# Optimization experiments

Measured on AMD Instinct MI355X. Metric: run time of the kernel, lower is better.

The kernel has to match this reference:

```python
import jax, jax.numpy as jnp
import numpy as np

TWO_PI = 6.283185  # constant used verbatim in the original module


def setup_inputs() -> dict:
    key = jax.random.key(0)
    ks = jax.random.split(key, 12)
    N, input_size, light_freq, H = 8388608, 11, 16, 16
    d_in = input_size - 2 + 2 * light_freq  # 41
    x = jax.random.uniform(ks[0], (N, input_size), dtype=jnp.float32)
    B_light = jax.random.normal(ks[1], (2, light_freq), dtype=jnp.float32)
    W1 = jax.random.normal(ks[2], (d_in, H), dtype=jnp.float32) * (1.0 / np.sqrt(d_in))
    b1 = jax.random.normal(ks[3], (H,), dtype=jnp.float32) * 0.01
    W2 = jax.random.normal(ks[4], (H, H), dtype=jnp.float32) * 0.25
    b2 = jax.random.normal(ks[5], (H,), dtype=jnp.float32) * 0.01
    W3 = jax.random.normal(ks[6], (H, H), dtype=jnp.float32) * 0.25
    b3 = jax.random.normal(ks[7], (H,), dtype=jnp.float32) * 0.01
    W4 = jax.random.normal(ks[8], (H, H), dtype=jnp.float32) * 0.25
    b4 = jax.random.normal(ks[9], (H,), dtype=jnp.float32) * 0.01
    W5 = jax.random.normal(ks[10], (H, 1), dtype=jnp.float32) * 0.25
    b5 = jax.random.normal(ks[11], (1,), dtype=jnp.float32) * 0.01
    return {"x": x, "B_light": B_light, "W1": W1, "b1": b1, "W2": W2, "b2": b2,
            "W3": W3, "b3": b3, "W4": W4, "b4": b4, "W5": W5, "b5": b5}


def reference(x, B_light, W1, b1, W2, b2, W3, b3, W4, b4, W5, b5):
    # Fourier-feature encoding of the last two input dims (light direction)
    x_light = TWO_PI * (x[:, -2:] @ B_light)                      # [N, F]
    feats = jnp.concatenate([x[:, :-2], jnp.cos(x_light), jnp.sin(x_light)], axis=-1)  # [N, 41]
    # Tiny 5-layer MLP with ELU activations
    h = jax.nn.elu(feats @ W1 + b1)
    h = jax.nn.elu(h @ W2 + b2)
    h = jax.nn.elu(h @ W3 + b3)
    h = jax.nn.elu(h @ W4 + b4)
    out = h @ W5 + b5                                             # [N, 1]
    return out
```

## Files before the change

kernel.cpp:

```cpp
#include <hip/hip_runtime.h>

typedef __fp16   cvt16x2 __attribute__((ext_vector_type(2)));
typedef _Float16 h2      __attribute__((ext_vector_type(2)));
typedef _Float16 half4_t __attribute__((ext_vector_type(4)));
typedef unsigned uint2v  __attribute__((ext_vector_type(2)));
typedef float    f32x4   __attribute__((ext_vector_type(4)));

#define CH 4

#if !__has_builtin(__builtin_elementwise_exp2)
extern "C" __device__ _Float16 __ocml_exp2_f16(_Float16);
#endif

__device__ __forceinline__ unsigned pk(float a, float b) {
    cvt16x2 h = __builtin_amdgcn_cvt_pkrtz(a, b);
    return __builtin_bit_cast(unsigned, h);
}
__device__ __forceinline__ half4_t mkfrag(unsigned lo, unsigned hi) {
    uint2v u; u[0] = lo; u[1] = hi;
    return __builtin_bit_cast(half4_t, u);
}

__device__ __forceinline__ unsigned elu_pk(float a, float b) {
    h2 v = __builtin_bit_cast(h2, __builtin_amdgcn_cvt_pkrtz(a, b));
    const h2 z  = {(_Float16)0.f, (_Float16)0.f};
    const h2 lg = {(_Float16)1.44269504f, (_Float16)1.44269504f};
    const h2 m1 = {(_Float16)-1.f, (_Float16)-1.f};
    h2 mx = __builtin_elementwise_max(v, z);
    h2 mn = __builtin_elementwise_min(v, z);
    h2 tt = mn * lg;
#if __has_builtin(__builtin_elementwise_exp2)
    h2 ev = __builtin_elementwise_exp2(tt);
#else
    h2 ev; ev[0] = __ocml_exp2_f16(tt[0]); ev[1] = __ocml_exp2_f16(tt[1]);
#endif
    h2 r = mx + (ev + m1);
    return __builtin_bit_cast(unsigned, r);
}

__device__ __forceinline__ float hdot2(unsigned a, unsigned b, float c) {
#if __has_builtin(__builtin_amdgcn_fdot2)
    return __builtin_amdgcn_fdot2(__builtin_bit_cast(cvt16x2, a),
                                  __builtin_bit_cast(cvt16x2, b), c, false);
#else
    h2 av = __builtin_bit_cast(h2, a), bv = __builtin_bit_cast(h2, b);
    return fmaf((float)av[1], (float)bv[1], fmaf((float)av[0], (float)bv[0], c));
#endif
}

__global__ __launch_bounds__(128, 4) void pixenc_mfma5(
    const float* __restrict__ x,
    const float* __restrict__ Bl,
    const float* __restrict__ W1, const float* __restrict__ b1,
    const float* __restrict__ W2, const float* __restrict__ b2,
    const float* __restrict__ W3, const float* __restrict__ b3,
    const float* __restrict__ W4, const float* __restrict__ b4,
    const float* __restrict__ W5, const float* __restrict__ b5,
    float* __restrict__ out, int N)
{
    const int t    = threadIdx.x;
    const int lane = t & 63;
    const int w    = t >> 6;
    const int g    = lane >> 4;
    const int m    = lane & 15;

    half4_t A1[3], A2, A3, A4;
    #pragma unroll
    for (int e = 0; e < 4; ++e) {
        const int c0 = 4 * e + g;
        A1[0][e] = (c0 < 9) ? (_Float16)W1[c0 * 16 + m] : (_Float16)0.f;
        A1[1][e] = (_Float16)W1[(9  + g * 4 + e) * 16 + m];
        A1[2][e] = (_Float16)W1[(25 + g * 4 + e) * 16 + m];
        A2[e]    = (_Float16)W2[(g * 4 + e) * 16 + m];
        A3[e]    = (_Float16)W3[(g * 4 + e) * 16 + m];
        A4[e]    = (_Float16)W4[(g * 4 + e) * 16 + m];
    }
    f32x4 c1, c2, c3, c4;
    float blc[4], bls[4];
    #pragma unroll
    for (int e = 0; e < 4; ++e) {
        const int r = g * 4 + e;
        c1[e] = b1[r]; c2[e] = b2[r]; c3[e] = b3[r]; c4[e] = b4[r];
        blc[e] = Bl[r]; bls[e] = Bl[16 + r];
    }
    const unsigned w5p0 = pk(W5[g * 4 + 0], W5[g * 4 + 1]);
    const unsigned w5p1 = pk(W5[g * 4 + 2], W5[g * 4 + 3]);
    const float b5v = b5[0];

    const int wavebase = blockIdx.x * (128 * CH) + w * (64 * CH);

    float xg0[4], xg1[4], x8v[4], x9v[4], x10v[4];
    #pragma unroll
    for (int s = 0; s < 4; ++s) {
        int j = wavebase + s * 16 + m; if (j >= N) j = N - 1;
        const float* rb = x + (size_t)j * 11;
        xg0[s] = rb[g];  xg1[s] = rb[4 + g];
        x8v[s] = rb[8];  x9v[s] = rb[9];  x10v[s] = rb[10];
    }

    #pragma unroll
    for (int c = 0; c < CH; ++c) {
        const int sbase = wavebase + c * 64;

        float ng0[4], ng1[4], n8[4], n9[4], n10[4];
        if (c + 1 < CH) {
            #pragma unroll
            for (int s = 0; s < 4; ++s) {
                int j = sbase + 64 + s * 16 + m; if (j >= N) j = N - 1;
                const float* rb = x + (size_t)j * 11;
                ng0[s] = rb[g];  ng1[s] = rb[4 + g];
                n8[s]  = rb[8];  n9[s]  = rb[9];  n10[s] = rb[10];
            }
        }

        f32x4 acc[4];
        #pragma unroll
        for (int s = 0; s < 4; ++s) {
            float cs[4], sn[4];
            #pragma unroll
            for (int e = 0; e < 4; ++e) {
                float zz = fmaf(x9v[s], blc[e], x10v[s] * bls[e]);
                zz = __builtin_amdgcn_fractf(zz);
                cs[e] = __builtin_amdgcn_cosf(zz);
                sn[e] = __builtin_amdgcn_sinf(zz);
            }
            const half4_t F0 = mkfrag(pk(xg0[s], xg1[s]), pk(x8v[s], 0.f));
            const half4_t F1 = mkfrag(pk(cs[0], cs[1]), pk(cs[2], cs[3]));
            const half4_t F2 = mkfrag(pk(sn[0], sn[1]), pk(sn[2], sn[3]));
            f32x4 a = c1;
            a = __builtin_amdgcn_mfma_f32_16x16x16f16(A1[0], F0, a, 0, 0, 0);
            a = __builtin_amdgcn_mfma_f32_16x16x16f16(A1[1], F1, a, 0, 0, 0);
            a = __builtin_amdgcn_mfma_f32_16x16x16f16(A1[2], F2, a, 0, 0, 0);
            acc[s] = a;
        }

        half4_t H[4];
        #pragma unroll
        for (int s = 0; s < 4; ++s)
            H[s] = mkfrag(elu_pk(acc[s][0], acc[s][1]), elu_pk(acc[s][2], acc[s][3]));
        #pragma unroll
        for (int s = 0; s < 4; ++s)
            acc[s] = __builtin_amdgcn_mfma_f32_16x16x16f16(A2, H[s], c2, 0, 0, 0);

        #pragma unroll
        for (int s = 0; s < 4; ++s)
            H[s] = mkfrag(elu_pk(acc[s][0], acc[s][1]), elu_pk(acc[s][2], acc[s][3]));
        #pragma unroll
        for (int s = 0; s < 4; ++s)
            acc[s] = __builtin_amdgcn_mfma_f32_16x16x16f16(A3, H[s], c3, 0, 0, 0);

        #pragma unroll
        for (int s = 0; s < 4; ++s)
            H[s] = mkfrag(elu_pk(acc[s][0], acc[s][1]), elu_pk(acc[s][2], acc[s][3]));
        #pragma unroll
        for (int s = 0; s < 4; ++s)
            acc[s] = __builtin_amdgcn_mfma_f32_16x16x16f16(A4, H[s], c4, 0, 0, 0);

        #pragma unroll
        for (int s = 0; s < 4; ++s) {
            const unsigned u0 = elu_pk(acc[s][0], acc[s][1]);
            const unsigned u1 = elu_pk(acc[s][2], acc[s][3]);
            float p = hdot2(u1, w5p1, hdot2(u0, w5p0, 0.f));
            p += __shfl_xor(p, 16, 64);
            p += __shfl_xor(p, 32, 64);
            const int o = sbase + s * 16 + m;
            if (g == 0 && o < N) out[o] = p + b5v;
        }

        if (c + 1 < CH) {
            #pragma unroll
            for (int s = 0; s < 4; ++s) {
                xg0[s] = ng0[s]; xg1[s] = ng1[s];
                x8v[s] = n8[s];  x9v[s] = n9[s];  x10v[s] = n10[s];
            }
        }
    }
}

extern "C" void kernel_launch(void* const* d_in, const int* in_sizes, int n_in,
                              void* d_out, int out_size, void* d_ws, size_t ws_size,
                              hipStream_t stream) {
    const float* x  = (const float*)d_in[0];
    const float* Bl = (const float*)d_in[1];
    const float* W1 = (const float*)d_in[2];
    const float* b1 = (const float*)d_in[3];
    const float* W2 = (const float*)d_in[4];
    const float* b2 = (const float*)d_in[5];
    const float* W3 = (const float*)d_in[6];
    const float* b3 = (const float*)d_in[7];
    const float* W4 = (const float*)d_in[8];
    const float* b4 = (const float*)d_in[9];
    const float* W5 = (const float*)d_in[10];
    const float* b5 = (const float*)d_in[11];
    float* out = (float*)d_out;

    const int N = out_size;
    const int blocks = (N + 128 * CH - 1) / (128 * CH);
    pixenc_mfma5<<<blocks, 128, 0, stream>>>(x, Bl, W1, b1, W2, b2, W3, b3,
                                             W4, b4, W5, b5, out, N);
}
```

Measured before the change: 144.9 us.

## Remove bounds checks via tail kernel, coalesce output stores, double chunk count

The main kernel now runs only on full blocks without per-row clamping, and a separate scalar kernel handles the remainder. Input addressing becomes strided pointer increments, and inputs are packed to fp16 at load time. After the shuffle reduction, each lane picks one sub-tile's result so all 64 lanes write one contiguous output instead of a quarter of lanes writing. ELU is simplified to max(v, exp(min(v,0))-1), and CH doubles to 8, halving the grid and amortising the weight setup per block at the cost of less parallelism.

```diff
diff --git a/kernel.cpp b/kernel.cpp
--- a/kernel.cpp
+++ b/kernel.cpp
@@ -6,7 +6,7 @@
 typedef unsigned uint2v  __attribute__((ext_vector_type(2)));
 typedef float    f32x4   __attribute__((ext_vector_type(4)));
 
-#define CH 4
+#define CH 8
 
 #if !__has_builtin(__builtin_elementwise_exp2)
 extern "C" __device__ _Float16 __ocml_exp2_f16(_Float16);
@@ -26,15 +26,13 @@
     const h2 z  = {(_Float16)0.f, (_Float16)0.f};
     const h2 lg = {(_Float16)1.44269504f, (_Float16)1.44269504f};
     const h2 m1 = {(_Float16)-1.f, (_Float16)-1.f};
-    h2 mx = __builtin_elementwise_max(v, z);
-    h2 mn = __builtin_elementwise_min(v, z);
-    h2 tt = mn * lg;
+    h2 t = __builtin_elementwise_min(v, z) * lg;
 #if __has_builtin(__builtin_elementwise_exp2)
-    h2 ev = __builtin_elementwise_exp2(tt);
+    h2 ev = __builtin_elementwise_exp2(t);
 #else
-    h2 ev; ev[0] = __ocml_exp2_f16(tt[0]); ev[1] = __ocml_exp2_f16(tt[1]);
+    h2 ev; ev[0] = __ocml_exp2_f16(t[0]); ev[1] = __ocml_exp2_f16(t[1]);
 #endif
-    h2 r = mx + (ev + m1);
+    h2 r = __builtin_elementwise_max(v, ev + m1);
     return __builtin_bit_cast(unsigned, r);
 }
 
@@ -48,7 +46,7 @@
 #endif
 }
 
-__global__ __launch_bounds__(128, 4) void pixenc_mfma5(
+__global__ __launch_bounds__(128, 4) void pixenc_mfma6(
     const float* __restrict__ x,
     const float* __restrict__ Bl,
     const float* __restrict__ W1, const float* __restrict__ b1,
@@ -56,7 +54,7 @@
     const float* __restrict__ W3, const float* __restrict__ b3,
     const float* __restrict__ W4, const float* __restrict__ b4,
     const float* __restrict__ W5, const float* __restrict__ b5,
-    float* __restrict__ out, int N)
+    float* __restrict__ out)
 {
     const int t    = threadIdx.x;
     const int lane = t & 63;
@@ -89,27 +87,32 @@
 
     const int wavebase = blockIdx.x * (128 * CH) + w * (64 * CH);
 
-    float xg0[4], xg1[4], x8v[4], x9v[4], x10v[4];
+    const float* aA = x + (size_t)(wavebase + m) * 11 + g;
+    const float* aB = x + (size_t)(wavebase + m) * 11 + 8;
+    float* outp = out + wavebase + lane;
+
+    unsigned cp0[4], cp8[4];
+    float cx9[4], cx10[4];
     #pragma unroll
     for (int s = 0; s < 4; ++s) {
-        int j = wavebase + s * 16 + m; if (j >= N) j = N - 1;
-        const float* rb = x + (size_t)j * 11;
-        xg0[s] = rb[g];  xg1[s] = rb[4 + g];
-        x8v[s] = rb[8];  x9v[s] = rb[9];  x10v[s] = rb[10];
+        const float a0 = aA[s * 176], a1 = aA[s * 176 + 4];
+        const float b8 = aB[s * 176], b9 = aB[s * 176 + 1], b10 = aB[s * 176 + 2];
+        cp0[s] = pk(a0, a1); cp8[s] = pk(b8, 0.f);
+        cx9[s] = b9; cx10[s] = b10;
     }
 
     #pragma unroll
     for (int c = 0; c < CH; ++c) {
-        const int sbase = wavebase + c * 64;
-
-        float ng0[4], ng1[4], n8[4], n9[4], n10[4];
+        unsigned np0[4], np8[4];
+        float nx9[4], nx10[4];
         if (c + 1 < CH) {
+            aA += 704; aB += 704;
             #pragma unroll
             for (int s = 0; s < 4; ++s) {
-                int j = sbase + 64 + s * 16 + m; if (j >= N) j = N - 1;
-                const float* rb = x + (size_t)j * 11;
-                ng0[s] = rb[g];  ng1[s] = rb[4 + g];
-                n8[s]  = rb[8];  n9[s]  = rb[9];  n10[s] = rb[10];
+                const float a0 = aA[s * 176], a1 = aA[s * 176 + 4];
+                const float b8 = aB[s * 176], b9 = aB[s * 176 + 1], b10 = aB[s * 176 + 2];
+                np0[s] = pk(a0, a1); np8[s] = pk(b8, 0.f);
+                nx9[s] = b9; nx10[s] = b10;
             }
         }
 
@@ -119,12 +122,12 @@
             float cs[4], sn[4];
             #pragma unroll
             for (int e = 0; e < 4; ++e) {
-                float zz = fmaf(x9v[s], blc[e], x10v[s] * bls[e]);
+                float zz = fmaf(cx9[s], blc[e], cx10[s] * bls[e]);
                 zz = __builtin_amdgcn_fractf(zz);
                 cs[e] = __builtin_amdgcn_cosf(zz);
                 sn[e] = __builtin_amdgcn_sinf(zz);
             }
-            const half4_t F0 = mkfrag(pk(xg0[s], xg1[s]), pk(x8v[s], 0.f));
+            const half4_t F0 = mkfrag(cp0[s], cp8[s]);
             const half4_t F1 = mkfrag(pk(cs[0], cs[1]), pk(cs[2], cs[3]));
             const half4_t F2 = mkfrag(pk(sn[0], sn[1]), pk(sn[2], sn[3]));
             f32x4 a = c1;
@@ -156,25 +159,72 @@
         for (int s = 0; s < 4; ++s)
             acc[s] = __builtin_amdgcn_mfma_f32_16x16x16f16(A4, H[s], c4, 0, 0, 0);
 
+        float p[4];
         #pragma unroll
         for (int s = 0; s < 4; ++s) {
             const unsigned u0 = elu_pk(acc[s][0], acc[s][1]);
             const unsigned u1 = elu_pk(acc[s][2], acc[s][3]);
-            float p = hdot2(u1, w5p1, hdot2(u0, w5p0, 0.f));
-            p += __shfl_xor(p, 16, 64);
-            p += __shfl_xor(p, 32, 64);
-            const int o = sbase + s * 16 + m;
-            if (g == 0 && o < N) out[o] = p + b5v;
-        }
+            p[s] = hdot2(u1, w5p1, hdot2(u0, w5p0, 0.f));
+        }
+        #pragma unroll
+        for (int s = 0; s < 4; ++s) p[s] += __shfl_xor(p[s], 16, 64);
+        #pragma unroll
+        for (int s = 0; s < 4; ++s) p[s] += __shfl_xor(p[s], 32, 64);
+
+        const float v01 = (g & 1) ? p[1] : p[0];
+        const float v23 = (g & 1) ? p[3] : p[2];
+        const float v   = (g & 2) ? v23 : v01;
+        outp[c * 64] = v + b5v;
 
         if (c + 1 < CH) {
             #pragma unroll
             for (int s = 0; s < 4; ++s) {
-                xg0[s] = ng0[s]; xg1[s] = ng1[s];
-                x8v[s] = n8[s];  x9v[s] = n9[s];  x10v[s] = n10[s];
+                cp0[s] = np0[s]; cp8[s] = np8[s];
+                cx9[s] = nx9[s]; cx10[s] = nx10[s];
             }
         }
     }
+}
+
+__global__ void pixenc_tail(
+    const float* __restrict__ x, const float* __restrict__ Bl,
+    const float* __restrict__ W1, const float* __restrict__ b1,
+    const float* __restrict__ W2, const float* __restrict__ b2,
+    const float* __restrict__ W3, const float* __restrict__ b3,
+    const float* __restrict__ W4, const float* __restrict__ b4,
+    const float* __restrict__ W5, const float* __restrict__ b5,
+    float* __restrict__ out, int N, int start)
+{
+    const int i = start + blockIdx.x * 256 + threadIdx.x;
+    if (i >= N) return;
+    const float* xr = x + (size_t)i * 11;
+    float feats[41];
+    for (int k = 0; k < 9; ++k) feats[k] = xr[k];
+    for (int f = 0; f < 16; ++f) {
+        const float ang = 6.283185f * (xr[9] * Bl[f] + xr[10] * Bl[16 + f]);
+        float s, c; __sincosf(ang, &s, &c);
+        feats[9 + f] = c; feats[25 + f] = s;
+    }
+    float h[16], gg[16];
+    for (int j = 0; j < 16; ++j) h[j] = b1[j];
+    for (int k = 0; k < 41; ++k)
+        for (int j = 0; j < 16; ++j) h[j] = fmaf(feats[k], W1[k * 16 + j], h[j]);
+    for (int j = 0; j < 16; ++j) h[j] = h[j] > 0.f ? h[j] : __expf(h[j]) - 1.f;
+    for (int j = 0; j < 16; ++j) gg[j] = b2[j];
+    for (int k = 0; k < 16; ++k)
+        for (int j = 0; j < 16; ++j) gg[j] = fmaf(h[k], W2[k * 16 + j], gg[j]);
+    for (int j = 0; j < 16; ++j) gg[j] = gg[j] > 0.f ? gg[j] : __expf(gg[j]) - 1.f;
+    for (int j = 0; j < 16; ++j) h[j] = b3[j];
+    for (int k = 0; k < 16; ++k)
+        for (int j = 0; j < 16; ++j) h[j] = fmaf(gg[k], W3[k * 16 + j], h[j]);
+    for (int j = 0; j < 16; ++j) h[j] = h[j] > 0.f ? h[j] : __expf(h[j]) - 1.f;
+    for (int j = 0; j < 16; ++j) gg[j] = b4[j];
+    for (int k = 0; k < 16; ++k)
+        for (int j = 0; j < 16; ++j) gg[j] = fmaf(h[k], W4[k * 16 + j], gg[j]);
+    for (int j = 0; j < 16; ++j) gg[j] = gg[j] > 0.f ? gg[j] : __expf(gg[j]) - 1.f;
+    float o = b5[0];
+    for (int j = 0; j < 16; ++j) o = fmaf(gg[j], W5[j], o);
+    out[i] = o;
 }
 
 extern "C" void kernel_launch(void* const* d_in, const int* in_sizes, int n_in,
@@ -195,7 +245,12 @@
     float* out = (float*)d_out;
 
     const int N = out_size;
-    const int blocks = (N + 128 * CH - 1) / (128 * CH);
-    pixenc_mfma5<<<blocks, 128, 0, stream>>>(x, Bl, W1, b1, W2, b2, W3, b3,
-                                             W4, b4, W5, b5, out, N);
-}
+    const int NB = N / (128 * CH);
+    const int rem = N - NB * (128 * CH);
+    if (NB > 0)
+        pixenc_mfma6<<<NB, 128, 0, stream>>>(x, Bl, W1, b1, W2, b2, W3, b3,
+                                             W4, b4, W5, b5, out);
+    if (rem > 0)
+        pixenc_tail<<<(rem + 255) / 256, 256, 0, stream>>>(
+            x, Bl, W1, b1, W2, b2, W3, b3, W4, b4, W5, b5, out, N, NB * 128 * CH);
+}
```

New measurement: 137.7 us. 1.05x faster.
